# Kernel optimization log

Hardware: AMD Instinct MI355X
Metric: run time of the kernel (lower is better)

## Reference

```python
import jax, jax.numpy as jnp
import numpy as np

V, N, C, DIM, DSPAN, H = 200000, 16384, 16, 300, 512, 150


def setup_inputs() -> dict:
    key = jax.random.key(0)
    ks = jax.random.split(key, 6)
    span_vecs = jax.random.normal(ks[0], (1, N, DSPAN), jnp.float32)
    candidates = jax.random.randint(ks[1], (1, N, C), 0, V)
    # binary candidate mask; guarantee every span has at least one candidate
    mask = (jax.random.uniform(ks[2], (1, N, C)) > 0.3).astype(jnp.float32)
    mask = mask.at[..., 0].set(1.0)
    embed_table = jax.random.normal(ks[3], (V, DIM), jnp.float32) * 0.1
    W1 = jax.random.normal(ks[4], (DSPAN + DIM, H), jnp.float32) * (1.0 / np.sqrt(DSPAN + DIM))
    b1 = jnp.zeros((H,), jnp.float32)
    W2 = jax.random.normal(ks[5], (H, 1), jnp.float32) * (1.0 / np.sqrt(H))
    b2 = jnp.zeros((1,), jnp.float32)
    return dict(span_vecs=span_vecs, candidates=candidates, mask_candidates=mask,
                embed_table=embed_table, W1=W1, b1=b1, W2=W2, b2=b2)


def reference(span_vecs, candidates, mask_candidates, embed_table, W1, b1, W2, b2):
    # gather candidate entity embeddings: [N, C, dim]
    cand_emb = embed_table[candidates[0]]
    sv = span_vecs[0]                                  # [N, Dspan]
    n, c = cand_emb.shape[0], cand_emb.shape[1]
    spans_exp = jnp.broadcast_to(sv[:, None, :], (n, c, sv.shape[-1]))
    ment = jnp.concatenate([spans_exp, cand_emb], axis=-1)  # [N, C, Dspan+dim]
    # 2-layer attention MLP scorer
    h = jax.nn.relu(ment @ W1 + b1)                    # [N, C, H]
    scores = (h @ W2 + b2)[..., 0]                     # [N, C]
    # masked softmax over candidates (log(0) = -inf masks out)
    scores = jax.nn.softmax(scores + jnp.log(mask_candidates[0]), axis=-1)
    # weighted sum of candidate embeddings
    weighted = jnp.einsum('ncd,nc->nd', cand_emb, scores)   # [N, dim]
    # pad span_vecs with dim zeros then scatter weighted into last dim slots
    # == concat since every span has candidates here
    out = jnp.concatenate([sv, weighted], axis=-1)[None]    # [1, N, Dspan+dim]
    return out
```

## Files before the change

kernel.cpp:

```cpp
#include <hip/hip_runtime.h>
#include <hip/hip_bf16.h>
#include <math.h>

#define NSPANS 16384
#define CC     16
#define DIM    300
#define DSPAN  512
#define HH     150
#define HP     160
#define DMENT  812
#define KP     320

typedef short bf16x8 __attribute__((ext_vector_type(8)));
typedef float f32x4  __attribute__((ext_vector_type(4)));

__device__ __forceinline__ unsigned short f2bf(float f) {
    union { float f; unsigned int u; } v; v.f = f;
    unsigned int r = (v.u + 0x7FFFu + ((v.u >> 16) & 1u)) >> 16;
    return (unsigned short)r;
}

__global__ __launch_bounds__(256) void k0_prep(const float* __restrict__ W1,
                                               unsigned short* __restrict__ Wt) {
    int idx = blockIdx.x * 256 + threadIdx.x;
    int n = idx / KP, k = idx - n * KP;
    float v = (n < HH && k < DIM) ? W1[(size_t)(DSPAN + k) * HH + n] : 0.f;
    Wt[idx] = f2bf(v);
}

__global__ __launch_bounds__(256) void k1_span(const float* __restrict__ sv,
                                               const float* __restrict__ W1,
                                               const float* __restrict__ b1,
                                               float* __restrict__ out) {
    const int b  = blockIdx.x;
    const int t  = threadIdx.x;
    const int n0 = b * 32;

    __shared__ float svc_t[32][36];
    __shared__ float w1c[32][HP];

    #pragma unroll
    for (int i = 0; i < 16; ++i) {
        int idx4 = t + i * 256;
        int r = idx4 >> 7, c4 = idx4 & 127;
        float4 v = *(const float4*)(sv + (size_t)(n0 + r) * DSPAN + c4 * 4);
        *(float4*)(out + (size_t)(n0 + r) * DMENT + c4 * 4) = v;
    }

    const int tc = t & 31;
    const int tr = t >> 5;
    const int j0 = tc * 5;
    const int r0 = tr * 4;

    float acc[4][5];
    #pragma unroll
    for (int i = 0; i < 4; ++i)
        #pragma unroll
        for (int j = 0; j < 5; ++j) acc[i][j] = 0.f;

    for (int k0 = 0; k0 < DSPAN; k0 += 32) {
        __syncthreads();
        {
            int r = t >> 3, c4 = t & 7;
            float4 v = *(const float4*)(sv + (size_t)(n0 + r) * DSPAN + k0 + c4 * 4);
            svc_t[c4 * 4 + 0][r] = v.x;
            svc_t[c4 * 4 + 1][r] = v.y;
            svc_t[c4 * 4 + 2][r] = v.z;
            svc_t[c4 * 4 + 3][r] = v.w;
        }
        #pragma unroll
        for (int i = 0; i < 20; ++i) {
            int idx = t + i * 256;
            int k = idx / HP, j = idx - (idx / HP) * HP;
            w1c[k][j] = (j < HH) ? W1[(size_t)(k0 + k) * HH + j] : 0.f;
        }
        __syncthreads();
        #pragma unroll
        for (int kk = 0; kk < 32; ++kk) {
            float4 a4 = *(const float4*)&svc_t[kk][r0];
            #pragma unroll
            for (int j = 0; j < 5; ++j) {
                float w = w1c[kk][j0 + j];
                acc[0][j] += a4.x * w;
                acc[1][j] += a4.y * w;
                acc[2][j] += a4.z * w;
                acc[3][j] += a4.w * w;
            }
        }
    }

    #pragma unroll
    for (int i = 0; i < 4; ++i)
        #pragma unroll
        for (int j = 0; j < 5; ++j) {
            int jj = j0 + j;
            if (jj < HH)
                out[(size_t)(n0 + r0 + i) * DMENT + DSPAN + jj] = acc[i][j] + b1[jj];
        }
}

__global__ __launch_bounds__(256) void k2_mfma(const int*   __restrict__ cand,
                                               const float* __restrict__ mask,
                                               const float* __restrict__ emb,
                                               const unsigned short* __restrict__ Wt,
                                               const float* __restrict__ W2,
                                               float*       __restrict__ out) {
    const int b  = blockIdx.x;
    const int t  = threadIdx.x;
    const int n0 = b * 16;
    const int w  = t >> 6;
    const int l  = t & 63;
    const int sp = l & 15;
    const int g  = l >> 4;

    __shared__ unsigned short A_lds[256][72];
    __shared__ unsigned short B_lds[160][72];
    __shared__ float hsL[16][HP];
    __shared__ float w2L[HP];
    __shared__ int   candL[256];
    __shared__ float maskL[256];
    __shared__ float scoresL[256];
    __shared__ float pL[256];

    candL[t] = cand[n0 * CC + t];
    maskL[t] = mask[n0 * CC + t];
    #pragma unroll
    for (int i = 0; i < 10; ++i) {
        int idx = t + i * 256;
        int s = idx / HP, j = idx - (idx / HP) * HP;
        hsL[s][j] = (j < HH) ? out[(size_t)(n0 + s) * DMENT + DSPAN + j] : 0.f;
    }
    if (t < HP) w2L[t] = (t < HH) ? W2[t] : 0.f;
    __syncthreads();

    const float* asrc = emb + (size_t)candL[t] * DIM;

    f32x4 acc[4][10];
    #pragma unroll
    for (int rt = 0; rt < 4; ++rt)
        #pragma unroll
        for (int nt = 0; nt < 10; ++nt) acc[rt][nt] = 0.f;

    for (int k0 = 0; k0 < KP; k0 += 64) {
        __syncthreads();
        if (k0 + 64 <= DIM) {
            #pragma unroll
            for (int q = 0; q < 8; ++q) {
                float4 v0 = *(const float4*)(asrc + k0 + q * 8);
                float4 v1 = *(const float4*)(asrc + k0 + q * 8 + 4);
                uint4 p;
                p.x = f2bf(v0.x) | ((unsigned)f2bf(v0.y) << 16);
                p.y = f2bf(v0.z) | ((unsigned)f2bf(v0.w) << 16);
                p.z = f2bf(v1.x) | ((unsigned)f2bf(v1.y) << 16);
                p.w = f2bf(v1.z) | ((unsigned)f2bf(v1.w) << 16);
                *(uint4*)&A_lds[t][q * 8] = p;
            }
        } else {
            #pragma unroll
            for (int q = 0; q < 8; ++q) {
                unsigned short e[8];
                #pragma unroll
                for (int i2 = 0; i2 < 8; ++i2) {
                    int kg = k0 + q * 8 + i2;
                    e[i2] = (kg < DIM) ? f2bf(asrc[kg]) : (unsigned short)0;
                }
                uint4 p;
                p.x = e[0] | ((unsigned)e[1] << 16);
                p.y = e[2] | ((unsigned)e[3] << 16);
                p.z = e[4] | ((unsigned)e[5] << 16);
                p.w = e[6] | ((unsigned)e[7] << 16);
                *(uint4*)&A_lds[t][q * 8] = p;
            }
        }
        #pragma unroll
        for (int i2 = 0; i2 < 5; ++i2) {
            int idx = t + i2 * 256;
            int row = idx >> 3, seg = idx & 7;
            uint4 v = *(const uint4*)(Wt + (size_t)row * KP + k0 + seg * 8);
            *(uint4*)&B_lds[row][seg * 8] = v;
        }
        __syncthreads();
        #pragma unroll
        for (int ks = 0; ks < 2; ++ks) {
            int koff = ks * 32 + g * 8;
            bf16x8 af[4];
            #pragma unroll
            for (int rt = 0; rt < 4; ++rt)
                af[rt] = *(const bf16x8*)&A_lds[w * 64 + rt * 16 + sp][koff];
            #pragma unroll
            for (int nt = 0; nt < 10; ++nt) {
                bf16x8 bfr = *(const bf16x8*)&B_lds[nt * 16 + sp][koff];
                #pragma unroll
                for (int rt = 0; rt < 4; ++rt)
                    acc[rt][nt] = __builtin_amdgcn_mfma_f32_16x16x32_bf16(af[rt], bfr, acc[rt][nt], 0, 0, 0);
            }
        }
    }

    #pragma unroll
    for (int rt = 0; rt < 4; ++rt) {
        int s = 4 * w + rt;
        float p0 = 0.f, p1 = 0.f, p2 = 0.f, p3 = 0.f;
        #pragma unroll
        for (int nt = 0; nt < 10; ++nt) {
            int col = nt * 16 + sp;
            float hb  = hsL[s][col];
            float w2v = w2L[col];
            p0 += fmaxf(acc[rt][nt][0] + hb, 0.f) * w2v;
            p1 += fmaxf(acc[rt][nt][1] + hb, 0.f) * w2v;
            p2 += fmaxf(acc[rt][nt][2] + hb, 0.f) * w2v;
            p3 += fmaxf(acc[rt][nt][3] + hb, 0.f) * w2v;
        }
        #pragma unroll
        for (int m = 1; m < 16; m <<= 1) {
            p0 += __shfl_xor(p0, m, 64);
            p1 += __shfl_xor(p1, m, 64);
            p2 += __shfl_xor(p2, m, 64);
            p3 += __shfl_xor(p3, m, 64);
        }
        if (sp == 0) {
            scoresL[s * 16 + g * 4 + 0] = p0;
            scoresL[s * 16 + g * 4 + 1] = p1;
            scoresL[s * 16 + g * 4 + 2] = p2;
            scoresL[s * 16 + g * 4 + 3] = p3;
        }
    }
    __syncthreads();

    {
        float v = (maskL[t] > 0.f) ? scoresL[t] : -INFINITY;
        float mx = v;
        #pragma unroll
        for (int m = 1; m < 16; m <<= 1) mx = fmaxf(mx, __shfl_xor(mx, m, 64));
        float e = expf(v - mx);
        float sm = e;
        #pragma unroll
        for (int m = 1; m < 16; m <<= 1) sm += __shfl_xor(sm, m, 64);
        pL[t] = e / sm;
    }
    __syncthreads();

    for (int idx = t; idx < 16 * 75; idx += 256) {
        int s = idx / 75, q = idx - s * 75;
        float4 a = make_float4(0.f, 0.f, 0.f, 0.f);
        #pragma unroll
        for (int c = 0; c < CC; ++c) {
            float p = pL[s * CC + c];
            float4 v = *(const float4*)(emb + (size_t)candL[s * CC + c] * DIM + q * 4);
            a.x += p * v.x; a.y += p * v.y; a.z += p * v.z; a.w += p * v.w;
        }
        *(float4*)(out + (size_t)(n0 + s) * DMENT + DSPAN + q * 4) = a;
    }
}

extern "C" void kernel_launch(void* const* d_in, const int* in_sizes, int n_in,
                              void* d_out, int out_size, void* d_ws, size_t ws_size,
                              hipStream_t stream) {
    const float* sv   = (const float*)d_in[0];
    const int*   cand = (const int*)d_in[1];
    const float* mask = (const float*)d_in[2];
    const float* emb  = (const float*)d_in[3];
    const float* W1   = (const float*)d_in[4];
    const float* b1   = (const float*)d_in[5];
    const float* W2   = (const float*)d_in[6];
    float* out = (float*)d_out;
    unsigned short* Wt = (unsigned short*)d_ws;

    k0_prep<<<(HP * KP) / 256, 256, 0, stream>>>(W1, Wt);
    k1_span<<<NSPANS / 32, 256, 0, stream>>>(sv, W1, b1, out);
    k2_mfma<<<NSPANS / 16, 256, 0, stream>>>(cand, mask, emb, Wt, W2, out);
}
```

Before: 659.3 us.

## Restructure candidate MLP kernel: one span per wave, register A fragments, full-K LDS weights

Each block now handles 8 spans with 512 threads, one wavefront per span. The whole bf16 W1 slice is staged in LDS once with a padded stride, and each lane loads its candidate embedding fragments straight from global memory into registers, with no A-tile LDS staging and no per-K-step barriers. Softmax is done within the wave using shuffles, and the weighted sum is computed per wave. The aim is to remove repeated synchronisation and LDS round-trips, at the cost of a large LDS footprint (about 105 KB per block), which may limit occupancy, and less reuse of the B fragments per MFMA.

```diff
diff --git a/kernel.cpp b/kernel.cpp
--- a/kernel.cpp
+++ b/kernel.cpp
@@ -10,6 +10,7 @@
 #define HP     160
 #define DMENT  812
 #define KP     320
+#define BSTR   328
 
 typedef short bf16x8 __attribute__((ext_vector_type(8)));
 typedef float f32x4  __attribute__((ext_vector_type(4)));
@@ -99,7 +100,7 @@
         }
 }
 
-__global__ __launch_bounds__(256) void k2_mfma(const int*   __restrict__ cand,
+__global__ __launch_bounds__(512) void k2_mfma(const int*   __restrict__ cand,
                                                const float* __restrict__ mask,
                                                const float* __restrict__ emb,
                                                const unsigned short* __restrict__ Wt,
@@ -107,149 +108,121 @@
                                                float*       __restrict__ out) {
     const int b  = blockIdx.x;
     const int t  = threadIdx.x;
-    const int n0 = b * 16;
+    const int n0 = b * 8;
     const int w  = t >> 6;
     const int l  = t & 63;
     const int sp = l & 15;
     const int g  = l >> 4;
 
-    __shared__ unsigned short A_lds[256][72];
-    __shared__ unsigned short B_lds[160][72];
-    __shared__ float hsL[16][HP];
+    __shared__ unsigned short B_lds[160][BSTR];
+    __shared__ float hsL[8][HP];
     __shared__ float w2L[HP];
-    __shared__ int   candL[256];
-    __shared__ float maskL[256];
-    __shared__ float scoresL[256];
-    __shared__ float pL[256];
-
-    candL[t] = cand[n0 * CC + t];
-    maskL[t] = mask[n0 * CC + t];
-    #pragma unroll
-    for (int i = 0; i < 10; ++i) {
-        int idx = t + i * 256;
-        int s = idx / HP, j = idx - (idx / HP) * HP;
+    __shared__ int   candL[128];
+    __shared__ float maskL[128];
+    __shared__ float pL[8][16];
+
+    if (t < 128) {
+        candL[t] = cand[n0 * CC + t];
+        maskL[t] = mask[n0 * CC + t];
+    }
+    for (int idx = t; idx < 8 * HP; idx += 512) {
+        int s = idx / HP, j = idx - s * HP;
         hsL[s][j] = (j < HH) ? out[(size_t)(n0 + s) * DMENT + DSPAN + j] : 0.f;
     }
     if (t < HP) w2L[t] = (t < HH) ? W2[t] : 0.f;
+    for (int idx = t; idx < 6400; idx += 512) {
+        int row = idx / 40, seg = idx - row * 40;
+        uint4 v = *(const uint4*)(Wt + (size_t)row * KP + seg * 8);
+        *(uint4*)&B_lds[row][seg * 8] = v;
+    }
     __syncthreads();
 
-    const float* asrc = emb + (size_t)candL[t] * DIM;
-
-    f32x4 acc[4][10];
-    #pragma unroll
-    for (int rt = 0; rt < 4; ++rt)
-        #pragma unroll
-        for (int nt = 0; nt < 10; ++nt) acc[rt][nt] = 0.f;
-
-    for (int k0 = 0; k0 < KP; k0 += 64) {
-        __syncthreads();
-        if (k0 + 64 <= DIM) {
-            #pragma unroll
-            for (int q = 0; q < 8; ++q) {
-                float4 v0 = *(const float4*)(asrc + k0 + q * 8);
-                float4 v1 = *(const float4*)(asrc + k0 + q * 8 + 4);
-                uint4 p;
-                p.x = f2bf(v0.x) | ((unsigned)f2bf(v0.y) << 16);
-                p.y = f2bf(v0.z) | ((unsigned)f2bf(v0.w) << 16);
-                p.z = f2bf(v1.x) | ((unsigned)f2bf(v1.y) << 16);
-                p.w = f2bf(v1.z) | ((unsigned)f2bf(v1.w) << 16);
-                *(uint4*)&A_lds[t][q * 8] = p;
-            }
-        } else {
-            #pragma unroll
-            for (int q = 0; q < 8; ++q) {
-                unsigned short e[8];
-                #pragma unroll
-                for (int i2 = 0; i2 < 8; ++i2) {
-                    int kg = k0 + q * 8 + i2;
-                    e[i2] = (kg < DIM) ? f2bf(asrc[kg]) : (unsigned short)0;
-                }
-                uint4 p;
-                p.x = e[0] | ((unsigned)e[1] << 16);
-                p.y = e[2] | ((unsigned)e[3] << 16);
-                p.z = e[4] | ((unsigned)e[5] << 16);
-                p.w = e[6] | ((unsigned)e[7] << 16);
-                *(uint4*)&A_lds[t][q * 8] = p;
-            }
-        }
-        #pragma unroll
-        for (int i2 = 0; i2 < 5; ++i2) {
-            int idx = t + i2 * 256;
-            int row = idx >> 3, seg = idx & 7;
-            uint4 v = *(const uint4*)(Wt + (size_t)row * KP + k0 + seg * 8);
-            *(uint4*)&B_lds[row][seg * 8] = v;
-        }
-        __syncthreads();
-        #pragma unroll
-        for (int ks = 0; ks < 2; ++ks) {
-            int koff = ks * 32 + g * 8;
-            bf16x8 af[4];
-            #pragma unroll
-            for (int rt = 0; rt < 4; ++rt)
-                af[rt] = *(const bf16x8*)&A_lds[w * 64 + rt * 16 + sp][koff];
-            #pragma unroll
-            for (int nt = 0; nt < 10; ++nt) {
-                bf16x8 bfr = *(const bf16x8*)&B_lds[nt * 16 + sp][koff];
-                #pragma unroll
-                for (int rt = 0; rt < 4; ++rt)
-                    acc[rt][nt] = __builtin_amdgcn_mfma_f32_16x16x32_bf16(af[rt], bfr, acc[rt][nt], 0, 0, 0);
-            }
-        }
-    }
-
-    #pragma unroll
-    for (int rt = 0; rt < 4; ++rt) {
-        int s = 4 * w + rt;
-        float p0 = 0.f, p1 = 0.f, p2 = 0.f, p3 = 0.f;
+    const float* asrc = emb + (size_t)candL[w * 16 + sp] * DIM;
+
+    float4 a[10][2];
+    #pragma unroll
+    for (int kt = 0; kt < 10; ++kt)
+        #pragma unroll
+        for (int h = 0; h < 2; ++h) {
+            int kb = kt * 32 + g * 8 + h * 4;
+            a[kt][h] = (kb < DIM) ? *(const float4*)(asrc + kb)
+                                  : make_float4(0.f, 0.f, 0.f, 0.f);
+        }
+
+    f32x4 acc[10];
+    #pragma unroll
+    for (int nt = 0; nt < 10; ++nt) acc[nt] = 0.f;
+
+    #pragma unroll
+    for (int kt = 0; kt < 10; ++kt) {
+        union { uint4 u; bf16x8 h; } cv;
+        cv.u.x = f2bf(a[kt][0].x) | ((unsigned)f2bf(a[kt][0].y) << 16);
+        cv.u.y = f2bf(a[kt][0].z) | ((unsigned)f2bf(a[kt][0].w) << 16);
+        cv.u.z = f2bf(a[kt][1].x) | ((unsigned)f2bf(a[kt][1].y) << 16);
+        cv.u.w = f2bf(a[kt][1].z) | ((unsigned)f2bf(a[kt][1].w) << 16);
+        bf16x8 af = cv.h;
+        const int koff = kt * 32 + g * 8;
         #pragma unroll
         for (int nt = 0; nt < 10; ++nt) {
-            int col = nt * 16 + sp;
-            float hb  = hsL[s][col];
-            float w2v = w2L[col];
-            p0 += fmaxf(acc[rt][nt][0] + hb, 0.f) * w2v;
-            p1 += fmaxf(acc[rt][nt][1] + hb, 0.f) * w2v;
-            p2 += fmaxf(acc[rt][nt][2] + hb, 0.f) * w2v;
-            p3 += fmaxf(acc[rt][nt][3] + hb, 0.f) * w2v;
-        }
-        #pragma unroll
-        for (int m = 1; m < 16; m <<= 1) {
-            p0 += __shfl_xor(p0, m, 64);
-            p1 += __shfl_xor(p1, m, 64);
-            p2 += __shfl_xor(p2, m, 64);
-            p3 += __shfl_xor(p3, m, 64);
-        }
-        if (sp == 0) {
-            scoresL[s * 16 + g * 4 + 0] = p0;
-            scoresL[s * 16 + g * 4 + 1] = p1;
-            scoresL[s * 16 + g * 4 + 2] = p2;
-            scoresL[s * 16 + g * 4 + 3] = p3;
-        }
+            bf16x8 bfr = *(const bf16x8*)&B_lds[nt * 16 + sp][koff];
+            acc[nt] = __builtin_amdgcn_mfma_f32_16x16x32_bf16(af, bfr, acc[nt], 0, 0, 0);
+        }
+    }
+
+    float s0 = 0.f, s1 = 0.f, s2 = 0.f, s3 = 0.f;
+    #pragma unroll
+    for (int nt = 0; nt < 10; ++nt) {
+        int col = nt * 16 + sp;
+        float hb  = hsL[w][col];
+        float w2v = w2L[col];
+        s0 += fmaxf(acc[nt][0] + hb, 0.f) * w2v;
+        s1 += fmaxf(acc[nt][1] + hb, 0.f) * w2v;
+        s2 += fmaxf(acc[nt][2] + hb, 0.f) * w2v;
+        s3 += fmaxf(acc[nt][3] + hb, 0.f) * w2v;
+    }
+    #pragma unroll
+    for (int m = 1; m < 16; m <<= 1) {
+        s0 += __shfl_xor(s0, m, 64);
+        s1 += __shfl_xor(s1, m, 64);
+        s2 += __shfl_xor(s2, m, 64);
+        s3 += __shfl_xor(s3, m, 64);
+    }
+
+    float v0 = (maskL[w * 16 + g * 4 + 0] > 0.f) ? s0 : -INFINITY;
+    float v1 = (maskL[w * 16 + g * 4 + 1] > 0.f) ? s1 : -INFINITY;
+    float v2 = (maskL[w * 16 + g * 4 + 2] > 0.f) ? s2 : -INFINITY;
+    float v3 = (maskL[w * 16 + g * 4 + 3] > 0.f) ? s3 : -INFINITY;
+    float mx = fmaxf(fmaxf(v0, v1), fmaxf(v2, v3));
+    mx = fmaxf(mx, __shfl_xor(mx, 16, 64));
+    mx = fmaxf(mx, __shfl_xor(mx, 32, 64));
+    float e0 = expf(v0 - mx), e1 = expf(v1 - mx), e2 = expf(v2 - mx), e3 = expf(v3 - mx);
+    float sm = (e0 + e1) + (e2 + e3);
+    sm += __shfl_xor(sm, 16, 64);
+    sm += __shfl_xor(sm, 32, 64);
+    if (sp == 0) {
+        pL[w][g * 4 + 0] = e0 / sm;
+        pL[w][g * 4 + 1] = e1 / sm;
+        pL[w][g * 4 + 2] = e2 / sm;
+        pL[w][g * 4 + 3] = e3 / sm;
     }
     __syncthreads();
 
-    {
-        float v = (maskL[t] > 0.f) ? scoresL[t] : -INFINITY;
-        float mx = v;
-        #pragma unroll
-        for (int m = 1; m < 16; m <<= 1) mx = fmaxf(mx, __shfl_xor(mx, m, 64));
-        float e = expf(v - mx);
-        float sm = e;
-        #pragma unroll
-        for (int m = 1; m < 16; m <<= 1) sm += __shfl_xor(sm, m, 64);
-        pL[t] = e / sm;
-    }
-    __syncthreads();
-
-    for (int idx = t; idx < 16 * 75; idx += 256) {
-        int s = idx / 75, q = idx - s * 75;
-        float4 a = make_float4(0.f, 0.f, 0.f, 0.f);
+    float pr[16];
+    const float* rp[16];
+    #pragma unroll
+    for (int c = 0; c < CC; ++c) {
+        pr[c] = pL[w][c];
+        rp[c] = emb + (size_t)candL[w * 16 + c] * DIM;
+    }
+    for (int q = l; q < 75; q += 64) {
+        float4 acc4 = make_float4(0.f, 0.f, 0.f, 0.f);
         #pragma unroll
         for (int c = 0; c < CC; ++c) {
-            float p = pL[s * CC + c];
-            float4 v = *(const float4*)(emb + (size_t)candL[s * CC + c] * DIM + q * 4);
-            a.x += p * v.x; a.y += p * v.y; a.z += p * v.z; a.w += p * v.w;
-        }
-        *(float4*)(out + (size_t)(n0 + s) * DMENT + DSPAN + q * 4) = a;
+            float p = pr[c];
+            float4 v = *(const float4*)(rp[c] + q * 4);
+            acc4.x += p * v.x; acc4.y += p * v.y; acc4.z += p * v.z; acc4.w += p * v.w;
+        }
+        *(float4*)(out + (size_t)(n0 + w) * DMENT + DSPAN + q * 4) = acc4;
     }
 }
 
@@ -268,5 +241,5 @@
 
     k0_prep<<<(HP * KP) / 256, 256, 0, stream>>>(W1, Wt);
     k1_span<<<NSPANS / 32, 256, 0, stream>>>(sv, W1, b1, out);
-    k2_mfma<<<NSPANS / 16, 256, 0, stream>>>(cand, mask, emb, Wt, W2, out);
-}
+    k2_mfma<<<NSPANS / 8, 512, 0, stream>>>(cand, mask, emb, Wt, W2, out);
+}
```

Result: faster. 628.1 us (-4.7%).
